# Kernel optimization log

Measured on AMD Instinct MI355X. Metric: run time of the kernel, lower is better.

The kernel has to match this reference:

```python
import jax, jax.numpy as jnp
import numpy as np

HEAD_DIM = 128
BAND_BITS = (5, 4, 4, 3)
N_BANDS = len(BAND_BITS)
BAND = HEAD_DIM // N_BANDS  # 32
FP16_MAX = 65504.0


def _hadamard(n):
    H = np.array([[1.0]], dtype=np.float32)
    while H.shape[0] < n:
        H = np.block([[H, H], [H, -H]])
    return H


def _mobius_perm(n):
    # Mobius function mu(i) for i = 1..n via sieve
    mu = np.ones(n + 1, dtype=np.int64)
    is_prime = np.ones(n + 1, dtype=bool)
    for p in range(2, n + 1):
        if is_prime[p]:
            is_prime[2 * p::p] = False
            mu[p::p] *= -1
            sq = p * p
            if sq <= n:
                mu[sq::sq] = 0
    # stable reorder of the 0..n-1 coordinates by descending mu(i+1)
    perm = np.argsort(-mu[1:n + 1], kind='stable').astype(np.int32)
    inv = np.argsort(perm).astype(np.int32)
    return perm, inv

_H = jnp.asarray(_hadamard(HEAD_DIM))            # [128,128], symmetric, H@H = 128*I
_PERM, _INV_PERM = (jnp.asarray(p) for p in _mobius_perm(HEAD_DIM))


def _banded_quant_dequant(z):
    # z: [N, HEAD_DIM] in WHT+Mobius space. Per-row, per-band symmetric quantization.
    zb = z.reshape(-1, N_BANDS, BAND)                       # [N, 4, 32]
    qmax = jnp.asarray([2 ** (b - 1) - 1 for b in BAND_BITS], jnp.float32)  # [4]
    amax = jnp.max(jnp.abs(zb), axis=-1)                    # [N, 4]
    scale = jnp.where(amax > 0, amax / qmax, 1.0)           # [N, 4]
    q = jnp.clip(jnp.round(zb / scale[..., None]), -qmax[:, None], qmax[:, None])
    return (q * scale[..., None]).reshape(-1, HEAD_DIM)


def setup_inputs() -> dict:
    key = jax.random.key(0)
    k1, k2 = jax.random.split(key)
    x = jax.random.normal(k1, (2, 512, 5120), dtype=jnp.float32)
    W = jax.random.normal(k2, (5120, 5120), dtype=jnp.float32) * 0.02
    b = jnp.zeros((5120,), dtype=jnp.float32)
    return {"x": x, "W": W, "b": b}


def reference(x, W, b):
    # cache-miss path: linear projection (result = cross_attn proj of T5 context)
    y = jnp.einsum('bld,ed->ble', x, W) + b                 # [B, L, 5120]
    orig_shape = y.shape
    yf = y.reshape(-1, HEAD_DIM)                            # [B*L*n_heads, 128]
    # put(): WHT -> Mobius reorder -> banded quantize
    z = yf @ _H                                             # unnormalized WHT
    z = z[:, _PERM]
    z = _banded_quant_dequant(z)
    # get(): un-reorder -> inverse WHT (WHT then /head_dim) -> clamp/nan_to_num
    z = z[:, _INV_PERM]
    r = (z @ _H) / HEAD_DIM
    r = jnp.clip(r, -FP16_MAX, FP16_MAX)
    r = jnp.nan_to_num(r, nan=0.0)
    return r.reshape(orig_shape)
```

## Files before the change

### kernel.cpp

```cpp
#include <hip/hip_runtime.h>
#include <math.h>

#define HEAD 128
typedef _Float16 f16;
typedef _Float16 f16x8 __attribute__((ext_vector_type(8)));
typedef _Float16 f16x4 __attribute__((ext_vector_type(4)));
typedef float f32x4 __attribute__((ext_vector_type(4)));

constexpr int mu_of(int n) {
  int m = n, cnt = 0;
  for (int p = 2; p * p <= m; ++p) {
    if (m % p == 0) {
      m /= p; ++cnt;
      if (m % p == 0) return 0;
    }
  }
  if (m > 1) ++cnt;
  return (cnt & 1) ? -1 : 1;
}
constexpr int key_of(int idx) {
  int mu = mu_of(idx + 1);
  return mu == 1 ? 0 : (mu == 0 ? 1 : 2);
}
struct Tbl {
  int band[HEAD];
  float qm[HEAD];
};
constexpr Tbl make_tbl() {
  Tbl t{};
  constexpr float qv[4] = {15.f, 7.f, 7.f, 3.f};
  for (int p = 0; p < HEAD; ++p) {
    int kp = key_of(p);
    int rank = 0;
    for (int j = 0; j < HEAD; ++j) {
      int kj = key_of(j);
      if (kj < kp || (kj == kp && j < p)) ++rank;
    }
    t.band[p] = rank >> 5;
    t.qm[p] = qv[rank >> 5];
  }
  return t;
}
__constant__ Tbl g_tbl = make_tbl();

__global__ __launch_bounds__(256) void split64_2(
    const float* __restrict__ x, const float* __restrict__ W,
    f16* __restrict__ xh, f16* __restrict__ xl,
    f16* __restrict__ wh, f16* __restrict__ wl, int n4x, int n4tot) {
  int i = blockIdx.x * blockDim.x + threadIdx.x;
  if (i >= n4tot) return;
  const float* s;
  f16 *h, *l;
  int j;
  if (i < n4x) {
    s = x; h = xh; l = xl; j = i;
  } else {
    s = W; h = wh; l = wl; j = i - n4x;
  }
  float4 v = ((const float4*)s)[j];
  v.x *= 64.f; v.y *= 64.f; v.z *= 64.f; v.w *= 64.f;
  f16 hx = (f16)v.x, hy = (f16)v.y, hz = (f16)v.z, hw = (f16)v.w;
  f16 lx = (f16)(v.x - (float)hx);
  f16 ly = (f16)(v.y - (float)hy);
  f16 lz = (f16)(v.z - (float)hz);
  f16 lw = (f16)(v.w - (float)hw);
  f16x4 hv = {hx, hy, hz, hw};
  f16x4 lv = {lx, ly, lz, lw};
  *(f16x4*)(h + 4 * (size_t)j) = hv;
  *(f16x4*)(l + 4 * (size_t)j) = lv;
}

__device__ __forceinline__ void dma16(const f16* g, f16* l) {
  __builtin_amdgcn_global_load_lds(
      (const __attribute__((address_space(1))) unsigned int*)g,
      (__attribute__((address_space(3))) unsigned int*)l, 16, 0, 0);
}

__global__ __launch_bounds__(256) void gemm_f16split_db(
    const f16* __restrict__ Ah, const f16* __restrict__ Al,
    const f16* __restrict__ Bh, const f16* __restrict__ Bl,
    const float* __restrict__ bias, float* __restrict__ C0,
    float* __restrict__ Cp, int M, int N, int K, int nsplit) {
  __shared__ f16 sAh[2][4096];
  __shared__ f16 sAl[2][4096];
  __shared__ f16 sBh[2][4096];
  __shared__ f16 sBl[2][4096];

  const int tid = threadIdx.x;
  const int lane = tid & 63;
  const int wave = tid >> 6;
  const int wr = wave >> 1;
  const int wc = wave & 1;

  const int nbm = M >> 7;
  const int nbn = N >> 7;
  const int tiles = nbm * nbn;
  const int nwg = gridDim.x;
  int wgid = blockIdx.x;
  if ((nwg & 7) == 0) {
    const int cpx = nwg >> 3;
    wgid = (wgid & 7) * cpx + (wgid >> 3);
  }
  const int split = wgid / tiles;
  const int tix = wgid % tiles;
  const int mb = tix % nbm;
  const int nb = tix / nbm;
  const int m0 = mb * 128;
  const int n0 = nb * 128;
  const int Ks = K / nsplit;
  const int k_beg = split * Ks;

  const int rsel = wave * 16 + (lane & 15);
  const int ksel = (lane >> 4) * 8;
  const f16* pAh = Ah + (size_t)(m0 + rsel) * K + ksel;
  const f16* pAl = Al + (size_t)(m0 + rsel) * K + ksel;
  const f16* pBh = Bh + (size_t)(n0 + rsel) * K + ksel;
  const f16* pBl = Bl + (size_t)(n0 + rsel) * K + ksel;
  const size_t r64 = (size_t)64 * K;

  f32x4 acc[4][4];
#pragma unroll
  for (int i = 0; i < 4; ++i)
#pragma unroll
    for (int j = 0; j < 4; ++j) acc[i][j] = (f32x4){0.f, 0.f, 0.f, 0.f};

  auto stage = [&](int k0, int b) {
    dma16(pAh + k0, &sAh[b][wave * 512]);
    dma16(pAh + k0 + r64, &sAh[b][2048 + wave * 512]);
    dma16(pAl + k0, &sAl[b][wave * 512]);
    dma16(pAl + k0 + r64, &sAl[b][2048 + wave * 512]);
    dma16(pBh + k0, &sBh[b][wave * 512]);
    dma16(pBh + k0 + r64, &sBh[b][2048 + wave * 512]);
    dma16(pBl + k0, &sBl[b][wave * 512]);
    dma16(pBl + k0 + r64, &sBl[b][2048 + wave * 512]);
  };

  const int nt = Ks >> 5;
  stage(k_beg, 0);
  if (nt > 1) stage(k_beg + 32, 1);

  const int lb = lane * 8;
  const int ca = wr * 4 * 512;
  const int cb = wc * 4 * 512;

  for (int t = 0; t < nt; ++t) {
    if (t + 1 < nt) {
      asm volatile("s_waitcnt vmcnt(8)" ::: "memory");
    } else {
      asm volatile("s_waitcnt vmcnt(0)" ::: "memory");
    }
    __builtin_amdgcn_sched_barrier(0);
    __builtin_amdgcn_s_barrier();

    const int b = t & 1;
    f16x8 ah[4], al[4], bh[4], bl[4];
#pragma unroll
    for (int i = 0; i < 4; ++i) {
      ah[i] = *(const f16x8*)&sAh[b][ca + i * 512 + lb];
      al[i] = *(const f16x8*)&sAl[b][ca + i * 512 + lb];
      bh[i] = *(const f16x8*)&sBh[b][cb + i * 512 + lb];
      bl[i] = *(const f16x8*)&sBl[b][cb + i * 512 + lb];
    }
    asm volatile("s_waitcnt lgkmcnt(0)" ::: "memory");
    __builtin_amdgcn_sched_barrier(0);
    __builtin_amdgcn_s_barrier();

    if (t + 2 < nt) stage(k_beg + (t + 2) * 32, b);

    __builtin_amdgcn_s_setprio(1);
#pragma unroll
    for (int i = 0; i < 4; ++i)
#pragma unroll
      for (int j = 0; j < 4; ++j) {
        acc[i][j] = __builtin_amdgcn_mfma_f32_16x16x32_f16(ah[i], bh[j], acc[i][j], 0, 0, 0);
        acc[i][j] = __builtin_amdgcn_mfma_f32_16x16x32_f16(al[i], bh[j], acc[i][j], 0, 0, 0);
        acc[i][j] = __builtin_amdgcn_mfma_f32_16x16x32_f16(ah[i], bl[j], acc[i][j], 0, 0, 0);
      }
    __builtin_amdgcn_s_setprio(0);
  }

  const float inv = 1.f / 4096.f;
  const int frow = lane & 15;
  const int kq = lane >> 4;
  const size_t MN = (size_t)M * N;
  float* dst = (split == 0) ? C0 : (Cp + (size_t)(split - 1) * MN);
#pragma unroll
  for (int j = 0; j < 4; ++j) {
    const int col = n0 + wc * 64 + j * 16 + frow;
    const float bv = (split == 0) ? bias[col] : 0.f;
#pragma unroll
    for (int i = 0; i < 4; ++i) {
#pragma unroll
      for (int r = 0; r < 4; ++r) {
        const int row = m0 + wr * 64 + i * 16 + kq * 4 + r;
        dst[(size_t)row * N + col] = acc[i][j][r] * inv + bv;
      }
    }
  }
}

#define BM 128
#define BN 64
#define BKK 8
#define TM 8
#define TN 4

__global__ __launch_bounds__(256) void sgemm_nt(
    const float* __restrict__ A, const float* __restrict__ B,
    const float* __restrict__ bias, float* __restrict__ C,
    int M, int N, int K) {
  __shared__ float As[BKK][BM];
  __shared__ float Bs[BKK][BN];

  const int tid = threadIdx.x;
  const int tn = tid & 15;
  const int tm = tid >> 4;
  const int bx = blockIdx.x;
  const int by = blockIdx.y;

  const float* Ab = A + (size_t)by * BM * K;
  const float* Bb = B + (size_t)bx * BN * K;

  const int ar = tid >> 1;
  const int ak = (tid & 1) * 4;

  float acc[TM][TN];
#pragma unroll
  for (int i = 0; i < TM; ++i)
#pragma unroll
    for (int j = 0; j < TN; ++j) acc[i][j] = 0.f;

  for (int k0 = 0; k0 < K; k0 += BKK) {
    float4 av = *(const float4*)(Ab + (size_t)ar * K + k0 + ak);
    float4 bv = make_float4(0.f, 0.f, 0.f, 0.f);
    if (tid < 128) bv = *(const float4*)(Bb + (size_t)ar * K + k0 + ak);

    __syncthreads();
    As[ak + 0][ar] = av.x;
    As[ak + 1][ar] = av.y;
    As[ak + 2][ar] = av.z;
    As[ak + 3][ar] = av.w;
    if (tid < 128) {
      Bs[ak + 0][ar] = bv.x;
      Bs[ak + 1][ar] = bv.y;
      Bs[ak + 2][ar] = bv.z;
      Bs[ak + 3][ar] = bv.w;
    }
    __syncthreads();

#pragma unroll
    for (int kk = 0; kk < BKK; ++kk) {
      float a[TM], b[TN];
#pragma unroll
      for (int i = 0; i < TM; ++i) a[i] = As[kk][tm * TM + i];
#pragma unroll
      for (int j = 0; j < TN; ++j) b[j] = Bs[kk][tn * TN + j];
#pragma unroll
      for (int i = 0; i < TM; ++i)
#pragma unroll
        for (int j = 0; j < TN; ++j) acc[i][j] += a[i] * b[j];
    }
  }

  const int row0 = by * BM + tm * TM;
  const int col0 = bx * BN + tn * TN;
  float bj[TN];
#pragma unroll
  for (int j = 0; j < TN; ++j) bj[j] = bias[col0 + j];
#pragma unroll
  for (int i = 0; i < TM; ++i) {
    float4 v = make_float4(acc[i][0] + bj[0], acc[i][1] + bj[1],
                           acc[i][2] + bj[2], acc[i][3] + bj[3]);
    *(float4*)(C + (size_t)(row0 + i) * N + col0) = v;
  }
}

__device__ inline void fwht2(float& e0, float& e1, int lane) {
  float a = e0 + e1;
  float b = e0 - e1;
  e0 = a;
  e1 = b;
#pragma unroll
  for (int s = 1; s <= 32; s <<= 1) {
    float p0 = __shfl_xor(e0, s);
    float p1 = __shfl_xor(e1, s);
    bool up = (lane & s) != 0;
    e0 = up ? (p0 - e0) : (e0 + p0);
    e1 = up ? (p1 - e1) : (e1 + p1);
  }
}

__global__ __launch_bounds__(256) void hadq(const float* __restrict__ Y,
                                            const float* __restrict__ P,
                                            int npart, float* __restrict__ O,
                                            int nrows) {
  const int lane = threadIdx.x & 63;
  const int wave = (blockIdx.x * (blockDim.x >> 6)) + (threadIdx.x >> 6);
  const int nwaves = gridDim.x * (blockDim.x >> 6);

  const int b0 = g_tbl.band[lane];
  const int b1 = g_tbl.band[lane + 64];
  const float qm0 = g_tbl.qm[lane];
  const float qm1 = g_tbl.qm[lane + 64];
  const size_t MN = (size_t)nrows * HEAD;

  for (int row = wave; row < nrows; row += nwaves) {
    const float* y = Y + (size_t)row * HEAD;
    float e0 = y[lane];
    float e1 = y[lane + 64];
    for (int p = 0; p < npart; ++p) {
      const float* pp = P + (size_t)p * MN + (size_t)row * HEAD;
      e0 += pp[lane];
      e1 += pp[lane + 64];
    }

    fwht2(e0, e1, lane);

    float f0 = fabsf(e0), f1 = fabsf(e1);
    float ab0 = fmaxf(b0 == 0 ? f0 : 0.f, b1 == 0 ? f1 : 0.f);
    float ab1 = fmaxf(b0 == 1 ? f0 : 0.f, b1 == 1 ? f1 : 0.f);
    float ab2 = fmaxf(b0 == 2 ? f0 : 0.f, b1 == 2 ? f1 : 0.f);
    float ab3 = fmaxf(b0 == 3 ? f0 : 0.f, b1 == 3 ? f1 : 0.f);
#pragma unroll
    for (int s = 32; s >= 1; s >>= 1) {
      ab0 = fmaxf(ab0, __shfl_xor(ab0, s));
      ab1 = fmaxf(ab1, __shfl_xor(ab1, s));
      ab2 = fmaxf(ab2, __shfl_xor(ab2, s));
      ab3 = fmaxf(ab3, __shfl_xor(ab3, s));
    }
    float am0 = b0 == 0 ? ab0 : (b0 == 1 ? ab1 : (b0 == 2 ? ab2 : ab3));
    float am1 = b1 == 0 ? ab0 : (b1 == 1 ? ab1 : (b1 == 2 ? ab2 : ab3));

    float s0 = am0 > 0.f ? am0 / qm0 : 1.0f;
    float s1 = am1 > 0.f ? am1 / qm1 : 1.0f;

    float q0 = fminf(fmaxf(rintf(e0 / s0), -qm0), qm0);
    float q1 = fminf(fmaxf(rintf(e1 / s1), -qm1), qm1);
    e0 = q0 * s0;
    e1 = q1 * s1;

    fwht2(e0, e1, lane);
    float r0 = e0 * 0.0078125f;
    float r1 = e1 * 0.0078125f;
    if (r0 != r0) r0 = 0.f;
    if (r1 != r1) r1 = 0.f;
    r0 = fminf(fmaxf(r0, -65504.f), 65504.f);
    r1 = fminf(fmaxf(r1, -65504.f), 65504.f);

    float* o = O + (size_t)row * HEAD;
    o[lane] = r0;
    o[lane + 64] = r1;
  }
}

extern "C" void kernel_launch(void* const* d_in, const int* in_sizes, int n_in,
                              void* d_out, int out_size, void* d_ws, size_t ws_size,
                              hipStream_t stream) {
  const float* x = (const float*)d_in[0];
  const float* W = (const float*)d_in[1];
  const float* b = (const float*)d_in[2];
  float* out = (float*)d_out;

  const int N = in_sizes[2];
  const int K = N;
  const int M = in_sizes[0] / K;

  const size_t MK = (size_t)M * K;
  const size_t NK = (size_t)N * K;
  const size_t MN = (size_t)M * N;
  const size_t need = (MK + NK) * 2 * sizeof(f16);

  const int nrows = out_size / HEAD;

  if (ws_size >= need && (M % 128) == 0 && (N % 128) == 0 && (K % 64) == 0) {
    f16* xh = (f16*)d_ws;
    f16* xl = xh + MK;
    f16* wh = xl + MK;
    f16* wl = wh + NK;
    float* Cp = (float*)((char*)d_ws + need);

    int nsplit = 1;
    if (ws_size >= need + 3 * MN * sizeof(float) && (K % 128) == 0)
      nsplit = 4;
    else if (ws_size >= need + 1 * MN * sizeof(float) && (K % 64) == 0)
      nsplit = 2;

    const int n4x = (int)(MK / 4);
    const int n4tot = (int)((MK + NK) / 4);
    split64_2<<<(n4tot + 255) / 256, 256, 0, stream>>>(x, W, xh, xl, wh, wl,
                                                       n4x, n4tot);

    const int nwg = (M / 128) * (N / 128) * nsplit;
    gemm_f16split_db<<<nwg, 256, 0, stream>>>(xh, xl, wh, wl, b, out, Cp, M,
                                              N, K, nsplit);

    hadq<<<512, 256, 0, stream>>>(out, Cp, nsplit - 1, out, nrows);
  } else {
    dim3 grid(N / BN, M / BM);
    sgemm_nt<<<grid, 256, 0, stream>>>(x, W, b, out, M, N, K);
    hadq<<<512, 256, 0, stream>>>(out, (const float*)out, 0, out, nrows);
  }
}
```

Measured before the change: 427.0 us.

## Replace LDS-staged GEMM with direct global-to-register double-buffered loads

```diff
diff --git a/kernel.cpp b/kernel.cpp
--- a/kernel.cpp
+++ b/kernel.cpp
@@ -70,22 +70,11 @@
   *(f16x4*)(l + 4 * (size_t)j) = lv;
 }
 
-__device__ __forceinline__ void dma16(const f16* g, f16* l) {
-  __builtin_amdgcn_global_load_lds(
-      (const __attribute__((address_space(1))) unsigned int*)g,
-      (__attribute__((address_space(3))) unsigned int*)l, 16, 0, 0);
-}
-
-__global__ __launch_bounds__(256) void gemm_f16split_db(
+__global__ __launch_bounds__(256) void gemm_f16split_reg(
     const f16* __restrict__ Ah, const f16* __restrict__ Al,
     const f16* __restrict__ Bh, const f16* __restrict__ Bl,
     const float* __restrict__ bias, float* __restrict__ C0,
     float* __restrict__ Cp, int M, int N, int K, int nsplit) {
-  __shared__ f16 sAh[2][4096];
-  __shared__ f16 sAl[2][4096];
-  __shared__ f16 sBh[2][4096];
-  __shared__ f16 sBl[2][4096];
-
   const int tid = threadIdx.x;
   const int lane = tid & 63;
   const int wave = tid >> 6;
@@ -109,14 +98,15 @@
   const int n0 = nb * 128;
   const int Ks = K / nsplit;
   const int k_beg = split * Ks;
-
-  const int rsel = wave * 16 + (lane & 15);
-  const int ksel = (lane >> 4) * 8;
-  const f16* pAh = Ah + (size_t)(m0 + rsel) * K + ksel;
-  const f16* pAl = Al + (size_t)(m0 + rsel) * K + ksel;
-  const f16* pBh = Bh + (size_t)(n0 + rsel) * K + ksel;
-  const f16* pBl = Bl + (size_t)(n0 + rsel) * K + ksel;
-  const size_t r64 = (size_t)64 * K;
+  const int nt = Ks >> 5;
+
+  const int frow = lane & 15;
+  const int fk = (lane >> 4) * 8;
+  const f16* pa_h = Ah + (size_t)(m0 + wr * 64 + frow) * K + fk + k_beg;
+  const f16* pa_l = Al + (size_t)(m0 + wr * 64 + frow) * K + fk + k_beg;
+  const f16* pb_h = Bh + (size_t)(n0 + wc * 64 + frow) * K + fk + k_beg;
+  const f16* pb_l = Bl + (size_t)(n0 + wc * 64 + frow) * K + fk + k_beg;
+  const size_t r16 = (size_t)16 * K;
 
   f32x4 acc[4][4];
 #pragma unroll
@@ -124,50 +114,19 @@
 #pragma unroll
     for (int j = 0; j < 4; ++j) acc[i][j] = (f32x4){0.f, 0.f, 0.f, 0.f};
 
-  auto stage = [&](int k0, int b) {
-    dma16(pAh + k0, &sAh[b][wave * 512]);
-    dma16(pAh + k0 + r64, &sAh[b][2048 + wave * 512]);
-    dma16(pAl + k0, &sAl[b][wave * 512]);
-    dma16(pAl + k0 + r64, &sAl[b][2048 + wave * 512]);
-    dma16(pBh + k0, &sBh[b][wave * 512]);
-    dma16(pBh + k0 + r64, &sBh[b][2048 + wave * 512]);
-    dma16(pBl + k0, &sBl[b][wave * 512]);
-    dma16(pBl + k0 + r64, &sBl[b][2048 + wave * 512]);
+  auto loadset = [&](f16x8 (&ah)[4], f16x8 (&al)[4], f16x8 (&bh)[4],
+                     f16x8 (&bl)[4], int koff) {
+#pragma unroll
+    for (int i = 0; i < 4; ++i) {
+      ah[i] = *(const f16x8*)(pa_h + (size_t)i * r16 + koff);
+      al[i] = *(const f16x8*)(pa_l + (size_t)i * r16 + koff);
+      bh[i] = *(const f16x8*)(pb_h + (size_t)i * r16 + koff);
+      bl[i] = *(const f16x8*)(pb_l + (size_t)i * r16 + koff);
+    }
   };
 
-  const int nt = Ks >> 5;
-  stage(k_beg, 0);
-  if (nt > 1) stage(k_beg + 32, 1);
-
-  const int lb = lane * 8;
-  const int ca = wr * 4 * 512;
-  const int cb = wc * 4 * 512;
-
-  for (int t = 0; t < nt; ++t) {
-    if (t + 1 < nt) {
-      asm volatile("s_waitcnt vmcnt(8)" ::: "memory");
-    } else {
-      asm volatile("s_waitcnt vmcnt(0)" ::: "memory");
-    }
-    __builtin_amdgcn_sched_barrier(0);
-    __builtin_amdgcn_s_barrier();
-
-    const int b = t & 1;
-    f16x8 ah[4], al[4], bh[4], bl[4];
-#pragma unroll
-    for (int i = 0; i < 4; ++i) {
-      ah[i] = *(const f16x8*)&sAh[b][ca + i * 512 + lb];
-      al[i] = *(const f16x8*)&sAl[b][ca + i * 512 + lb];
-      bh[i] = *(const f16x8*)&sBh[b][cb + i * 512 + lb];
-      bl[i] = *(const f16x8*)&sBl[b][cb + i * 512 + lb];
-    }
-    asm volatile("s_waitcnt lgkmcnt(0)" ::: "memory");
-    __builtin_amdgcn_sched_barrier(0);
-    __builtin_amdgcn_s_barrier();
-
-    if (t + 2 < nt) stage(k_beg + (t + 2) * 32, b);
-
-    __builtin_amdgcn_s_setprio(1);
+  auto mfmaset = [&](f16x8 (&ah)[4], f16x8 (&al)[4], f16x8 (&bh)[4],
+                     f16x8 (&bl)[4]) {
 #pragma unroll
     for (int i = 0; i < 4; ++i)
 #pragma unroll
@@ -176,11 +135,20 @@
         acc[i][j] = __builtin_amdgcn_mfma_f32_16x16x32_f16(al[i], bh[j], acc[i][j], 0, 0, 0);
         acc[i][j] = __builtin_amdgcn_mfma_f32_16x16x32_f16(ah[i], bl[j], acc[i][j], 0, 0, 0);
       }
-    __builtin_amdgcn_s_setprio(0);
+  };
+
+  f16x8 a0h[4], a0l[4], b0h[4], b0l[4];
+  f16x8 a1h[4], a1l[4], b1h[4], b1l[4];
+
+  loadset(a0h, a0l, b0h, b0l, 0);
+  for (int t = 0; t < nt; t += 2) {
+    loadset(a1h, a1l, b1h, b1l, (t + 1) * 32);
+    mfmaset(a0h, a0l, b0h, b0l);
+    if (t + 2 < nt) loadset(a0h, a0l, b0h, b0l, (t + 2) * 32);
+    mfmaset(a1h, a1l, b1h, b1l);
   }
 
   const float inv = 1.f / 4096.f;
-  const int frow = lane & 15;
   const int kq = lane >> 4;
   const size_t MN = (size_t)M * N;
   float* dst = (split == 0) ? C0 : (Cp + (size_t)(split - 1) * MN);
@@ -380,9 +348,9 @@
     float* Cp = (float*)((char*)d_ws + need);
 
     int nsplit = 1;
-    if (ws_size >= need + 3 * MN * sizeof(float) && (K % 128) == 0)
+    if (ws_size >= need + 3 * MN * sizeof(float) && (K % 256) == 0)
       nsplit = 4;
-    else if (ws_size >= need + 1 * MN * sizeof(float) && (K % 64) == 0)
+    else if (ws_size >= need + 1 * MN * sizeof(float) && (K % 128) == 0)
       nsplit = 2;
 
     const int n4x = (int)(MK / 4);
@@ -391,8 +359,8 @@
                                                        n4x, n4tot);
 
     const int nwg = (M / 128) * (N / 128) * nsplit;
-    gemm_f16split_db<<<nwg, 256, 0, stream>>>(xh, xl, wh, wl, b, out, Cp, M,
-                                              N, K, nsplit);
+    gemm_f16split_reg<<<nwg, 256, 0, stream>>>(xh, xl, wh, wl, b, out, Cp,
+                                               M, N, K, nsplit);
 
     hadq<<<512, 256, 0, stream>>>(out, Cp, nsplit - 1, out, nrows);
   } else {
```

Result: slower. 592.0 us (+38.6%).
